# Kernel tuning notes

Measured on AMD Instinct MI355X. Metric: run time of the kernel, lower is better.

The kernel has to match this reference:

```python
import jax, jax.numpy as jnp
import numpy as np

B, L, DM = 4, 64, 1024
H, DK, DV = 16, 64, 64
D = H * DV            # 1024, selector feature dim
DI = 4096             # ffn hidden
NEG = -1.0e9


def _layer_norm(x, g, b, eps=1e-6):
    mu = jnp.mean(x, axis=-1, keepdims=True)
    var = jnp.mean((x - mu) ** 2, axis=-1, keepdims=True)
    return (x - mu) / jnp.sqrt(var + eps) * g + b


def setup_inputs() -> dict:
    key = jax.random.key(0)
    ks = jax.random.split(key, 20)
    s = 0.02
    inp = {
        'input_t': jax.random.normal(ks[0], (B, L, DM), jnp.float32),
        'input_a': jax.random.normal(ks[1], (B, L, DM), jnp.float32),
        'input_v': jax.random.normal(ks[2], (B, L, DM), jnp.float32),
        'mask': jnp.ones((B, L, L), jnp.int32),
        # attention projections (Linear without bias -> right-multiply matrices)
        'w_qs': jax.random.normal(ks[3], (DM, H * DK), jnp.float32) * s,
        'w_ks': jax.random.normal(ks[4], (DM, H * DK), jnp.float32) * s,
        'w_vs': jax.random.normal(ks[5], (DM, H * DV), jnp.float32) * s,
        'w_ds0': jax.random.normal(ks[6], (DM, D), jnp.float32) * s,
        'w_ds1': jax.random.normal(ks[7], (DM, D), jnp.float32) * s,
        # decision MLP dc: Linear(2D,2D) + ReLU + Linear(2D,2)
        'dc_w1': jax.random.normal(ks[8], (2 * D, 2 * D), jnp.float32) * s,
        'dc_b1': jnp.zeros((2 * D,), jnp.float32),
        'dc_w2': jax.random.normal(ks[9], (2 * D, 2), jnp.float32) * s,
        'dc_b2': jnp.zeros((2,), jnp.float32),
        'w_fc': jax.random.normal(ks[10], (H * DV, DM), jnp.float32) * s,
        'ln1_g': jnp.ones((DM,), jnp.float32),
        'ln1_b': jnp.zeros((DM,), jnp.float32),
        # shared positionwise FFN
        'ffn_w1': jax.random.normal(ks[11], (DM, DI), jnp.float32) * s,
        'ffn_b1': jnp.zeros((DI,), jnp.float32),
        'ffn_w2': jax.random.normal(ks[12], (DI, DM), jnp.float32) * s,
        'ffn_b2': jnp.zeros((DM,), jnp.float32),
        'ln2_g': jnp.ones((DM,), jnp.float32),
        'ln2_b': jnp.zeros((DM,), jnp.float32),
    }
    return inp


def _forward(input_t, input_a, input_v, mask, w_qs, w_ks, w_vs, w_ds0, w_ds1,
             dc_w1, dc_b1, dc_w2, dc_b2, w_fc, ln1_g, ln1_b,
             ffn_w1, ffn_b1, ffn_w2, ffn_b2, ln2_g, ln2_b):
    temp = DK ** 0.5
    lis = [input_t, input_a, input_v]
    nm = len(lis)
    mask4 = mask[:, None]  # [B,1,L,L], broadcast over heads
    outs = []
    for i in range(nm):  # query modality (fixed small loop)
        x = lis[i]
        residual = x
        d0 = x @ w_ds0                                      # [B,L,D]
        # f[b,q,k] = cat(d1[b,q], d0[b,k]); split dc_w1 rows to avoid [B,L,L,2D] input
        a0 = d0 @ dc_w1[D:]                                 # [B,L,2D] (key-index part)
        q = (x @ w_qs).reshape(B, L, H, DK).transpose(0, 2, 1, 3)  # [B,H,L,DK]
        attns, vs = [], []
        for j in range(nm):  # key/value modality
            y = lis[j]
            k = (y @ w_ks).reshape(B, L, H, DK).transpose(0, 2, 1, 3)
            v = (y @ w_vs).reshape(B, L, H, DV).transpose(0, 2, 1, 3)
            d1 = y @ w_ds1
            a1 = d1 @ dc_w1[:D]                              # [B,L,2D] (query-index part)
            hid = jax.nn.relu(a1[:, :, None, :] + a0[:, None, :, :] + dc_b1)  # [B,L,L,2D]
            logits = hid @ dc_w2 + dc_b2                     # [B,L,L,2]
            # gumbel_softmax, eval mode (no noise), tau=1, hard=True (straight-through)
            p = jax.nn.softmax(logits, axis=-1)
            y_soft = jax.nn.softmax(p, axis=-1)
            idx = jnp.argmax(y_soft, axis=-1)
            y_hard = jax.nn.one_hot(idx, 2, dtype=y_soft.dtype)
            ret = y_hard - jax.lax.stop_gradient(y_soft) + y_soft
            dec = ret[..., 1] * NEG                          # [B,L,L]
            attn = jnp.einsum('bhqd,bhkd->bhqk', q / temp, k) + dec[:, None]
            attn = jnp.where(mask4 == 0, NEG, attn)
            attns.append(attn)
            vs.append(v)
        A = jnp.stack(attns, axis=3).reshape(B, H, L, nm * L)  # [B,H,L,3L]
        A = jax.nn.softmax(A, axis=-1)
        V = jnp.stack(vs, axis=2).reshape(B, H, nm * L, DV)
        o = jnp.einsum('bhqk,bhkd->bhqd', A, V)
        o = o.transpose(0, 2, 1, 3).reshape(B, L, H * DV)
        o = o @ w_fc + residual
        o = _layer_norm(o, ln1_g, ln1_b)
        outs.append(o)
    # shared positionwise FFN applied to all modalities
    res = []
    for o in outs:
        h = jax.nn.relu(o @ ffn_w1 + ffn_b1) @ ffn_w2 + ffn_b2
        res.append(_layer_norm(h + o, ln2_g, ln2_b))
    return jnp.stack(res)  # [3,B,L,DM]


def reference(input_t, input_a, input_v, mask, w_qs, w_ks, w_vs, w_ds0, w_ds1,
              dc_w1, dc_b1, dc_w2, dc_b2, w_fc, ln1_g, ln1_b,
              ffn_w1, ffn_b1, ffn_w2, ffn_b2, ln2_g, ln2_b):
    return _forward(input_t, input_a, input_v, mask, w_qs, w_ks, w_vs, w_ds0, w_ds1,
                    dc_w1, dc_b1, dc_w2, dc_b2, w_fc, ln1_g, ln1_b,
                    ffn_w1, ffn_b1, ffn_w2, ffn_b2, ln2_g, ln2_b)
```

## Files before the change

kernel.cpp:

```cpp
#include <hip/hip_runtime.h>
#include <math.h>


#define NEGV (-1000000000.0f)

typedef float f32x4 __attribute__((ext_vector_type(4)));
typedef short short8 __attribute__((ext_vector_type(8)));
typedef unsigned short u16x8 __attribute__((ext_vector_type(8)));
typedef unsigned short u16x4 __attribute__((ext_vector_type(4)));

typedef __attribute__((address_space(1))) const void glob_cv;
typedef __attribute__((address_space(3))) void lds_v;

static __device__ __forceinline__ unsigned short f2bf(float f) {
  unsigned u = __builtin_bit_cast(unsigned, f);
  u += 0x7fffu + ((u >> 16) & 1u);
  return (unsigned short)(u >> 16);
}
static __device__ __forceinline__ float bf2f(unsigned short h) {
  return __builtin_bit_cast(float, ((unsigned)h) << 16);
}

static __device__ __forceinline__ void gload16(const unsigned short* g,
                                               unsigned short* l) {
  __builtin_amdgcn_global_load_lds((glob_cv*)g, (lds_v*)l, 16, 0, 0);
}

__global__ __launch_bounds__(256) void concat3(const float4* __restrict__ t,
                                               const float4* __restrict__ a,
                                               const float4* __restrict__ v,
                                               float4* __restrict__ Xf,
                                               u16x4* __restrict__ Xb) {
  int id = blockIdx.x * 256 + threadIdx.x;
  int m = id >> 16;
  int off = id & 65535;
  const float4* s = (m == 0) ? t : (m == 1) ? a : v;
  float4 val = s[off];
  Xf[id] = val;
  u16x4 bb;
  bb.x = f2bf(val.x); bb.y = f2bf(val.y);
  bb.z = f2bf(val.z); bb.w = f2bf(val.w);
  Xb[id] = bb;
}

struct WtJob { const float* src; unsigned short* dst; int K, N, tstart; };
struct WtJobs { WtJob j[9]; };

__global__ __launch_bounds__(256) void wt_transpose(WtJobs jobs) {
  __shared__ float Ls[32][33];
  int ji = 0;
#pragma unroll
  for (int t = 1; t < 9; ++t)
    if ((int)blockIdx.x >= jobs.j[t].tstart) ji = t;
  const WtJob jb = jobs.j[ji];
  int local = blockIdx.x - jb.tstart;
  int ntx = jb.N >> 5;
  int tk = local / ntx, tn = local - tk * ntx;
  const int tid = threadIdx.x;
  const int r = tid >> 3, c = (tid & 7) * 4;
  float4 v = *(const float4*)(jb.src + (size_t)(tk * 32 + r) * jb.N + tn * 32 + c);
  Ls[r][c + 0] = v.x; Ls[r][c + 1] = v.y;
  Ls[r][c + 2] = v.z; Ls[r][c + 3] = v.w;
  __syncthreads();
  u16x4 o;
  o.x = f2bf(Ls[c + 0][r]);
  o.y = f2bf(Ls[c + 1][r]);
  o.z = f2bf(Ls[c + 2][r]);
  o.w = f2bf(Ls[c + 3][r]);
  *(u16x4*)(jb.dst + (size_t)(tn * 32 + r) * jb.K + tk * 32 + c) = o;
}

struct GemmOp {
  const unsigned short* A;
  const unsigned short* B;
  const float* bias;
  const float* add;
  float* Cf;
  unsigned short* Cb;
  int lda, ldb, N, K, relu;
};
struct GemmBatch { GemmOp op[5]; };

__global__ __launch_bounds__(256, 2) void gemm_mfma(GemmBatch batch) {
  const GemmOp g = batch.op[blockIdx.z];
  __shared__ unsigned short As[64 * 64];
  __shared__ unsigned short Bs[128 * 64];
  const int bm = blockIdx.y * 64, bn = blockIdx.x * 128;
  const int tid = threadIdx.x;
  const int l = tid & 63, w = tid >> 6;
  const int wr = (w >> 1) * 32, wc = (w & 1) * 64;
  const int lr = l & 15, lg = l >> 4;
  const int crow = l >> 3;
  const int scol = ((l & 7) ^ (l >> 3)) * 8;
  const char* AsB = (const char*)As;
  const char* BsB = (const char*)Bs;
  f32x4 acc[2][4] = {};
  for (int k0 = 0; k0 < g.K; k0 += 64) {
    __syncthreads();
#pragma unroll
    for (int c = 0; c < 2; ++c) {
      const int ch = w * 2 + c;
      gload16(g.A + (size_t)(bm + ch * 8 + crow) * g.lda + k0 + scol,
              &As[ch * 512 + l * 8]);
    }
#pragma unroll
    for (int c = 0; c < 4; ++c) {
      const int ch = w * 4 + c;
      gload16(g.B + (size_t)(bn + ch * 8 + crow) * g.ldb + k0 + scol,
              &Bs[ch * 512 + l * 8]);
    }
    __syncthreads();
#pragma unroll
    for (int ks = 0; ks < 2; ++ks) {
      short8 af[2], bf[4];
#pragma unroll
      for (int i = 0; i < 2; ++i) {
        const int ra = wr + i * 16 + lr;
        af[i] = *(const short8*)(AsB +
                 ((ra * 128 + ks * 64 + lg * 16) ^ ((ra & 7) << 4)));
      }
#pragma unroll
      for (int j = 0; j < 4; ++j) {
        const int rb = wc + j * 16 + lr;
        bf[j] = *(const short8*)(BsB +
                 ((rb * 128 + ks * 64 + lg * 16) ^ ((rb & 7) << 4)));
      }
#pragma unroll
      for (int i = 0; i < 2; ++i)
#pragma unroll
        for (int j = 0; j < 4; ++j)
          acc[i][j] =
              __builtin_amdgcn_mfma_f32_16x16x32_bf16(af[i], bf[j], acc[i][j], 0, 0, 0);
    }
  }
#pragma unroll
  for (int j = 0; j < 4; ++j) {
    const int col = bn + wc + j * 16 + lr;
    const float bv = g.bias ? g.bias[col] : 0.0f;
#pragma unroll
    for (int i = 0; i < 2; ++i) {
#pragma unroll
      for (int ii = 0; ii < 4; ++ii) {
        const int row = bm + wr + i * 16 + lg * 4 + ii;
        float v = acc[i][j][ii] + bv;
        if (g.add) v += g.add[(size_t)row * g.N + col];
        if (g.relu) v = fmaxf(v, 0.0f);
        if (g.Cf) g.Cf[(size_t)row * g.N + col] = v;
        if (g.Cb) g.Cb[(size_t)row * g.N + col] = f2bf(v);
      }
    }
  }
}

__global__ __launch_bounds__(256) void decision_part(
    const float* __restrict__ A1, const float* __restrict__ A0,
    const float* __restrict__ w2, float* __restrict__ PART) {
  __shared__ float sA1[64][68];
  __shared__ float sA0[64][68];
  const int ds = blockIdx.x;
  const int b = blockIdx.y, pp = blockIdx.z;
  const int i = pp / 3, j = pp % 3;
  const int tid = threadIdx.x;
  const int tq = tid >> 4, tk = tid & 15;
  const float* a1base = A1 + ((size_t)(j * 4 + b) * 64) * 2048 + ds * 64;
  const float* a0base = A0 + ((size_t)(i * 4 + b) * 64) * 2048 + ds * 64;
#pragma unroll
  for (int t = 0; t < 4; ++t) {
    const int row = t * 16 + tq;
    const int col = tk * 4;
    *(float4*)&sA1[row][col] = *(const float4*)(a1base + (size_t)row * 2048 + col);
    *(float4*)&sA0[row][col] = *(const float4*)(a0base + (size_t)row * 2048 + col);
  }
  __syncthreads();
  float acc[4][4] = {};
  const float* wbase = w2 + (size_t)ds * 128;
#pragma unroll 4
  for (int s4 = 0; s4 < 16; ++s4) {
    float4 wv0 = *(const float4*)(wbase + s4 * 8);
    float4 wv1 = *(const float4*)(wbase + s4 * 8 + 4);
    float wd0 = wv0.y - wv0.x, wd1 = wv0.w - wv0.z;
    float wd2 = wv1.y - wv1.x, wd3 = wv1.w - wv1.z;
    float4 a1v[4], a0v[4];
#pragma unroll
    for (int r = 0; r < 4; ++r) {
      a1v[r] = *(const float4*)&sA1[tq + 16 * r][s4 * 4];
      a0v[r] = *(const float4*)&sA0[tk + 16 * r][s4 * 4];
    }
#pragma unroll
    for (int qr = 0; qr < 4; ++qr)
#pragma unroll
      for (int kr = 0; kr < 4; ++kr) {
        float a = acc[qr][kr];
        a = fmaf(fmaxf(a1v[qr].x + a0v[kr].x, 0.f), wd0, a);
        a = fmaf(fmaxf(a1v[qr].y + a0v[kr].y, 0.f), wd1, a);
        a = fmaf(fmaxf(a1v[qr].z + a0v[kr].z, 0.f), wd2, a);
        a = fmaf(fmaxf(a1v[qr].w + a0v[kr].w, 0.f), wd3, a);
        acc[qr][kr] = a;
      }
  }
  float* outp = PART + (size_t)ds * 147456 + ((size_t)pp * 4 + b) * 4096;
#pragma unroll
  for (int qr = 0; qr < 4; ++qr)
#pragma unroll
    for (int kr = 0; kr < 4; ++kr)
      outp[(tq + 16 * qr) * 64 + (tk + 16 * kr)] = acc[qr][kr];
}

__global__ __launch_bounds__(256) void decision_reduce(
    const float* __restrict__ PART, const float* __restrict__ b2,
    float* __restrict__ DEC) {
  const int out = blockIdx.x * 256 + threadIdx.x;
  float acc = 0.f;
#pragma unroll
  for (int s = 0; s < 32; ++s) acc += PART[(size_t)s * 147456 + out];
  const float thr = b2[0] - b2[1];
  DEC[out] = (acc > thr) ? NEGV : 0.f;
}

__global__ __launch_bounds__(256) void attn_mfma(
    const unsigned short* __restrict__ Qa, const unsigned short* __restrict__ Ka,
    const unsigned short* __restrict__ Va, const float* __restrict__ DEC,
    const int* __restrict__ mask, unsigned short* __restrict__ O) {
  __shared__ __align__(16) char sm[49408];
  char* KsP = sm;
  char* Vt = sm + 24576;
  float* invs = (float*)(sm + 49152);

  const int h = blockIdx.x, b = blockIdx.y, i = blockIdx.z;
  const int tid = threadIdx.x;
  const int l = tid & 63, w = tid >> 6;
  const int l15 = l & 15, lg = l >> 4;

#pragma unroll
  for (int rep = 0; rep < 6; ++rep) {
    int flat = rep * 256 + tid;
    int key = flat >> 3, c8 = flat & 7;
    int j = key >> 6, kl = key & 63;
    const size_t rowoff = (((size_t)(j * 4 + b) * 64 + kl) * 1024) + h * 64 + c8 * 8;
    u16x8 kv = *(const u16x8*)(Ka + rowoff);
    *(u16x8*)(KsP + ((key * 128 + c8 * 16) ^ ((key & 7) << 4))) = kv;
    u16x8 vv = *(const u16x8*)(Va + rowoff);
#pragma unroll
    for (int jj = 0; jj < 8; ++jj) {
      int d = c8 * 8 + jj;
      *(unsigned short*)(Vt + ((d * 384 + key * 2) ^ ((d & 7) << 4))) = vv[jj];
    }
  }

  const int qg = w * 16 + l15;
  const unsigned short* qsrc =
      Qa + (((size_t)(i * 4 + b) * 64 + qg) * 1024) + h * 64 + lg * 8;
  short8 qf0 = *(const short8*)(qsrc);
  short8 qf1 = *(const short8*)(qsrc + 32);

  __syncthreads();

  f32x4 s[12];
#pragma unroll
  for (int t = 0; t < 12; ++t) {
    const int key = t * 16 + l15;
    const int swz = (key & 7) << 4;
    short8 kf0 = *(const short8*)(KsP + ((key * 128 + 0 + lg * 16) ^ swz));
    short8 kf1 = *(const short8*)(KsP + ((key * 128 + 64 + lg * 16) ^ swz));
    f32x4 z = {0.f, 0.f, 0.f, 0.f};
    z = __builtin_amdgcn_mfma_f32_16x16x32_bf16(kf0, qf0, z, 0, 0, 0);
    z = __builtin_amdgcn_mfma_f32_16x16x32_bf16(kf1, qf1, z, 0, 0, 0);
    s[t] = z;
  }

  int mk[4][4];
#pragma unroll
  for (int t4 = 0; t4 < 4; ++t4)
#pragma unroll
    for (int r = 0; r < 4; ++r)
      mk[t4][r] = mask[((size_t)b * 64 + qg) * 64 + t4 * 16 + lg * 4 + r];

  float mx = -3.0e38f;
#pragma unroll
  for (int t = 0; t < 12; ++t) {
    const float* dbase =
        DEC + (((size_t)(i * 3 + (t >> 2)) * 4 + b) * 4096) + qg * 64;
#pragma unroll
    for (int r = 0; r < 4; ++r) {
      const int kl = (t & 3) * 16 + lg * 4 + r;
      float sv = s[t][r] * 0.125f + dbase[kl];
      if (mk[t & 3][r] == 0) sv = NEGV;
      s[t][r] = sv;
      mx = fmaxf(mx, sv);
    }
  }
  mx = fmaxf(mx, __shfl_xor(mx, 16));
  mx = fmaxf(mx, __shfl_xor(mx, 32));
  float sum = 0.f;
#pragma unroll
  for (int t = 0; t < 12; ++t)
#pragma unroll
    for (int r = 0; r < 4; ++r) {
      float p = __expf(s[t][r] - mx);
      s[t][r] = p;
      sum += p;
    }
  sum += __shfl_xor(sum, 16);
  sum += __shfl_xor(sum, 32);
  if (l < 16) invs[w * 16 + l] = 1.0f / sum;

  __syncthreads();

  char* Pmy = KsP + w * 6144;
  const int pswz = (l15 & 7) << 4;

#pragma unroll
  for (int t = 0; t < 12; ++t)
#pragma unroll
    for (int r = 0; r < 4; ++r) {
      const int key = t * 16 + lg * 4 + r;
      *(unsigned short*)(Pmy + ((l15 * 384 + key * 2) ^ pswz)) = f2bf(s[t][r]);
    }
  __syncthreads();

  f32x4 o[4] = {};
#pragma unroll
  for (int kc = 0; kc < 6; ++kc) {
    short8 pf = *(const short8*)(Pmy + ((l15 * 384 + kc * 64 + lg * 16) ^ pswz));
#pragma unroll
    for (int dt = 0; dt < 4; ++dt) {
      const int d = dt * 16 + l15;
      short8 vf = *(const short8*)(Vt + ((d * 384 + kc * 64 + lg * 16) ^ ((d & 7) << 4)));
      o[dt] = __builtin_amdgcn_mfma_f32_16x16x32_bf16(pf, vf, o[dt], 0, 0, 0);
    }
  }
  __syncthreads();

#pragma unroll
  for (int t = 0; t < 12; ++t)
#pragma unroll
    for (int r = 0; r < 4; ++r) {
      const int key = t * 16 + lg * 4 + r;
      float p = s[t][r];
      float lo = p - bf2f(f2bf(p));
      *(unsigned short*)(Pmy + ((l15 * 384 + key * 2) ^ pswz)) = f2bf(lo);
    }
  __syncthreads();

#pragma unroll
  for (int kc = 0; kc < 6; ++kc) {
    short8 pf = *(const short8*)(Pmy + ((l15 * 384 + kc * 64 + lg * 16) ^ pswz));
#pragma unroll
    for (int dt = 0; dt < 4; ++dt) {
      const int d = dt * 16 + l15;
      short8 vf = *(const short8*)(Vt + ((d * 384 + kc * 64 + lg * 16) ^ ((d & 7) << 4)));
      o[dt] = __builtin_amdgcn_mfma_f32_16x16x32_bf16(pf, vf, o[dt], 0, 0, 0);
    }
  }

#pragma unroll
  for (int dt = 0; dt < 4; ++dt)
#pragma unroll
    for (int r = 0; r < 4; ++r) {
      const int ql = lg * 4 + r;
      const float inv = invs[w * 16 + ql];
      const int d = dt * 16 + l15;
      O[(((size_t)(i * 4 + b) * 64 + w * 16 + ql) * 1024) + h * 64 + d] =
          f2bf(o[dt][r] * inv);
    }
}

__global__ __launch_bounds__(256) void ln_kernel(const float* __restrict__ X,
                                                 const float* __restrict__ g,
                                                 const float* __restrict__ be,
                                                 float* __restrict__ Y,
                                                 unsigned short* __restrict__ Yb) {
  __shared__ float rs[8];
  int row = blockIdx.x, tid = threadIdx.x;
  const float* x = X + (size_t)row * 1024 + tid * 4;
  float4 v = *(const float4*)x;
  float s = v.x + v.y + v.z + v.w;
  float s2 = v.x * v.x + v.y * v.y + v.z * v.z + v.w * v.w;
#pragma unroll
  for (int off = 32; off > 0; off >>= 1) {
    s += __shfl_down(s, off);
    s2 += __shfl_down(s2, off);
  }
  int lane = tid & 63, wid = tid >> 6;
  if (lane == 0) { rs[wid * 2] = s; rs[wid * 2 + 1] = s2; }
  __syncthreads();
  if (tid == 0) {
    float aa = rs[0] + rs[2] + rs[4] + rs[6];
    float cc = rs[1] + rs[3] + rs[5] + rs[7];
    rs[0] = aa; rs[1] = cc;
  }
  __syncthreads();
  float mu = rs[0] * (1.0f / 1024.0f);
  float var = rs[1] * (1.0f / 1024.0f) - mu * mu;
  var = fmaxf(var, 0.f);
  float inv = 1.0f / sqrtf(var + 1e-6f);
  float4 gv = *(const float4*)(g + tid * 4);
  float4 bv = *(const float4*)(be + tid * 4);
  float4 o;
  o.x = (v.x - mu) * inv * gv.x + bv.x;
  o.y = (v.y - mu) * inv * gv.y + bv.y;
  o.z = (v.z - mu) * inv * gv.z + bv.z;
  o.w = (v.w - mu) * inv * gv.w + bv.w;
  *(float4*)(Y + (size_t)row * 1024 + tid * 4) = o;
  if (Yb) {
    u16x4 ob;
    ob.x = f2bf(o.x); ob.y = f2bf(o.y); ob.z = f2bf(o.z); ob.w = f2bf(o.w);
    *(u16x4*)(Yb + (size_t)row * 1024 + tid * 4) = ob;
  }
}

__global__ __launch_bounds__(256) void fsum_ln(
    const float* __restrict__ P, const float* __restrict__ bias,
    const float* __restrict__ add, const float* __restrict__ g,
    const float* __restrict__ be, float* __restrict__ Y) {
  __shared__ float rs[8];
  int row = blockIdx.x, tid = threadIdx.x;
  const int c = tid * 4;
  const size_t o = (size_t)row * 1024 + c;
  float4 p0 = *(const float4*)(P + o);
  float4 p1 = *(const float4*)(P + 786432 + o);
  float4 p2 = *(const float4*)(P + 2 * 786432 + o);
  float4 p3 = *(const float4*)(P + 3 * 786432 + o);
  float4 bs = *(const float4*)(bias + c);
  float4 ad = *(const float4*)(add + o);
  float4 v;
  v.x = ((p0.x + p1.x) + (p2.x + p3.x)) + bs.x + ad.x;
  v.y = ((p0.y + p1.y) + (p2.y + p3.y)) + bs.y + ad.y;
  v.z = ((p0.z + p1.z) + (p2.z + p3.z)) + bs.z + ad.z;
  v.w = ((p0.w + p1.w) + (p2.w + p3.w)) + bs.w + ad.w;
  float s = v.x + v.y + v.z + v.w;
  float s2 = v.x * v.x + v.y * v.y + v.z * v.z + v.w * v.w;
#pragma unroll
  for (int off = 32; off > 0; off >>= 1) {
    s += __shfl_down(s, off);
    s2 += __shfl_down(s2, off);
  }
  int lane = tid & 63, wid = tid >> 6;
  if (lane == 0) { rs[wid * 2] = s; rs[wid * 2 + 1] = s2; }
  __syncthreads();
  if (tid == 0) {
    float aa = rs[0] + rs[2] + rs[4] + rs[6];
    float cc = rs[1] + rs[3] + rs[5] + rs[7];
    rs[0] = aa; rs[1] = cc;
  }
  __syncthreads();
  float mu = rs[0] * (1.0f / 1024.0f);
  float var = rs[1] * (1.0f / 1024.0f) - mu * mu;
  var = fmaxf(var, 0.f);
  float inv = 1.0f / sqrtf(var + 1e-6f);
  float4 gv = *(const float4*)(g + c);
  float4 bv = *(const float4*)(be + c);
  float4 r;
  r.x = (v.x - mu) * inv * gv.x + bv.x;
  r.y = (v.y - mu) * inv * gv.y + bv.y;
  r.z = (v.z - mu) * inv * gv.z + bv.z;
  r.w = (v.w - mu) * inv * gv.w + bv.w;
  *(float4*)(Y + o) = r;
}

extern "C" void kernel_launch(void* const* d_in, const int* in_sizes, int n_in,
                              void* d_out, int out_size, void* d_ws,
                              size_t ws_size, hipStream_t stream) {
  const float* in_t = (const float*)d_in[0];
  const float* in_a = (const float*)d_in[1];
  const float* in_v = (const float*)d_in[2];
  const int* mask = (const int*)d_in[3];
  const float* w_qs = (const float*)d_in[4];
  const float* w_ks = (const float*)d_in[5];
  const float* w_vs = (const float*)d_in[6];
  const float* w_ds0 = (const float*)d_in[7];
  const float* w_ds1 = (const float*)d_in[8];
  const float* dc_w1 = (const float*)d_in[9];
  const float* dc_b1 = (const float*)d_in[10];
  const float* dc_w2 = (const float*)d_in[11];
  const float* dc_b2 = (const float*)d_in[12];
  const float* w_fc = (const float*)d_in[13];
  const float* ln1_g = (const float*)d_in[14];
  const float* ln1_b = (const float*)d_in[15];
  const float* ffn_w1 = (const float*)d_in[16];
  const float* ffn_b1 = (const float*)d_in[17];
  const float* ffn_w2 = (const float*)d_in[18];
  const float* ffn_b2 = (const float*)d_in[19];
  const float* ln2_g = (const float*)d_in[20];
  const float* ln2_b = (const float*)d_in[21];
  float* out = (float*)d_out;

  char* p = (char*)d_ws;
  auto alloc = [&](size_t bytes) {
    char* r = p;
    p += (bytes + 255) & ~(size_t)255;
    return r;
  };
  unsigned short* WQS = (unsigned short*)alloc(1024 * 1024 * 2);
  unsigned short* WKS = (unsigned short*)alloc(1024 * 1024 * 2);
  unsigned short* WVS = (unsigned short*)alloc(1024 * 1024 * 2);
  unsigned short* WD0 = (unsigned short*)alloc(1024 * 1024 * 2);
  unsigned short* WD1 = (unsigned short*)alloc(1024 * 1024 * 2);
  unsigned short* WW1 = (unsigned short*)alloc((size_t)2048 * 2048 * 2);
  unsigned short* WFC = (unsigned short*)alloc(1024 * 1024 * 2);
  unsigned short* WF1 = (unsigned short*)alloc((size_t)4096 * 1024 * 2);
  unsigned short* WF2 = (unsigned short*)alloc((size_t)1024 * 4096 * 2);
  float* Xf = (float*)alloc((size_t)786432 * 4);
  unsigned short* Xb = (unsigned short*)alloc((size_t)786432 * 2);
  unsigned short* Qb = (unsigned short*)alloc((size_t)786432 * 2);
  unsigned short* Kb = (unsigned short*)alloc((size_t)786432 * 2);
  unsigned short* Vb = (unsigned short*)alloc((size_t)786432 * 2);
  unsigned short* D0b = (unsigned short*)alloc((size_t)786432 * 2);
  unsigned short* D1b = (unsigned short*)alloc((size_t)786432 * 2);
  float* DEC = (float*)alloc((size_t)147456 * 4);
  unsigned short* OATTb = (unsigned short*)alloc((size_t)786432 * 2);
  float* PART = (float*)alloc((size_t)32 * 147456 * 4);
  float* FPART = PART;
  char* U = alloc((size_t)14155776);
  float* A0f = (float*)U;
  float* A1f = (float*)(U + (size_t)6291456);
  float* F2 = (float*)U;
  float* O1f = (float*)(U + (size_t)3145728);
  unsigned short* O1b = (unsigned short*)(U + (size_t)6291456);
  unsigned short* Hfb = (unsigned short*)(U + (size_t)7864320);

  dim3 blk(256);

  WtJobs jobs;
  int ts = 0;
  auto setjob = [&](int idx, const float* s, unsigned short* d, int K, int N) {
    jobs.j[idx].src = s; jobs.j[idx].dst = d;
    jobs.j[idx].K = K; jobs.j[idx].N = N; jobs.j[idx].tstart = ts;
    ts += (K / 32) * (N / 32);
  };
  setjob(0, w_qs, WQS, 1024, 1024);
  setjob(1, w_ks, WKS, 1024, 1024);
  setjob(2, w_vs, WVS, 1024, 1024);
  setjob(3, w_ds0, WD0, 1024, 1024);
  setjob(4, w_ds1, WD1, 1024, 1024);
  setjob(5, dc_w1, WW1, 2048, 2048);
  setjob(6, w_fc, WFC, 1024, 1024);
  setjob(7, ffn_w1, WF1, 1024, 4096);
  setjob(8, ffn_w2, WF2, 4096, 1024);
  wt_transpose<<<dim3(ts), blk, 0, stream>>>(jobs);

  concat3<<<dim3(768), blk, 0, stream>>>((const float4*)in_t,
                                         (const float4*)in_a,
                                         (const float4*)in_v,
                                         (float4*)Xf, (u16x4*)Xb);

  GemmBatch proj{};
  unsigned short* pouts[5] = {Qb, Kb, Vb, D0b, D1b};
  const unsigned short* pws[5] = {WQS, WKS, WVS, WD0, WD1};
  for (int z = 0; z < 5; ++z) {
    proj.op[z].A = Xb; proj.op[z].B = pws[z];
    proj.op[z].bias = nullptr; proj.op[z].add = nullptr;
    proj.op[z].Cf = nullptr; proj.op[z].Cb = pouts[z];
    proj.op[z].lda = 1024; proj.op[z].ldb = 1024;
    proj.op[z].N = 1024; proj.op[z].K = 1024; proj.op[z].relu = 0;
  }
  gemm_mfma<<<dim3(8, 12, 5), blk, 0, stream>>>(proj);

  GemmBatch pair{};
  pair.op[0].A = D0b; pair.op[0].B = WW1 + 1024;
  pair.op[0].bias = nullptr; pair.op[0].add = nullptr;
  pair.op[0].Cf = A0f; pair.op[0].Cb = nullptr;
  pair.op[0].lda = 1024; pair.op[0].ldb = 2048;
  pair.op[0].N = 2048; pair.op[0].K = 1024; pair.op[0].relu = 0;
  pair.op[1] = pair.op[0];
  pair.op[1].A = D1b; pair.op[1].B = WW1; pair.op[1].bias = dc_b1;
  pair.op[1].Cf = A1f;
  gemm_mfma<<<dim3(16, 12, 2), blk, 0, stream>>>(pair);

  decision_part<<<dim3(32, 4, 9), blk, 0, stream>>>(A1f, A0f, dc_w2, PART);
  decision_reduce<<<dim3(576), blk, 0, stream>>>(PART, dc_b2, DEC);

  attn_mfma<<<dim3(16, 4, 3), blk, 0, stream>>>(Qb, Kb, Vb, DEC, mask, OATTb);

  GemmBatch fc{};
  fc.op[0].A = OATTb; fc.op[0].B = WFC;
  fc.op[0].bias = nullptr; fc.op[0].add = Xf;
  fc.op[0].Cf = F2; fc.op[0].Cb = nullptr;
  fc.op[0].lda = 1024; fc.op[0].ldb = 1024;
  fc.op[0].N = 1024; fc.op[0].K = 1024; fc.op[0].relu = 0;
  gemm_mfma<<<dim3(8, 12, 1), blk, 0, stream>>>(fc);

  ln_kernel<<<dim3(768), blk, 0, stream>>>(F2, ln1_g, ln1_b, O1f, O1b);

  GemmBatch f1{};
  f1.op[0].A = O1b; f1.op[0].B = WF1;
  f1.op[0].bias = ffn_b1; f1.op[0].add = nullptr;
  f1.op[0].Cf = nullptr; f1.op[0].Cb = Hfb;
  f1.op[0].lda = 1024; f1.op[0].ldb = 1024;
  f1.op[0].N = 4096; f1.op[0].K = 1024; f1.op[0].relu = 1;
  gemm_mfma<<<dim3(32, 12, 1), blk, 0, stream>>>(f1);

  GemmBatch f2{};
  for (int z = 0; z < 4; ++z) {
    f2.op[z].A = Hfb + (size_t)z * 1024;
    f2.op[z].B = WF2 + (size_t)z * 1024;
    f2.op[z].bias = nullptr; f2.op[z].add = nullptr;
    f2.op[z].Cf = FPART + (size_t)z * 786432; f2.op[z].Cb = nullptr;
    f2.op[z].lda = 4096; f2.op[z].ldb = 4096;
    f2.op[z].N = 1024; f2.op[z].K = 1024; f2.op[z].relu = 0;
  }
  gemm_mfma<<<dim3(8, 12, 4), blk, 0, stream>>>(f2);

  fsum_ln<<<dim3(768), blk, 0, stream>>>(FPART, ffn_b2, O1f, ln2_g, ln2_b, out);
}
```

Measured before the change: 163.0 us.

## Double-buffer GEMM LDS tiles and merge concat and weight transpose kernels

The GEMM kernel now keeps two LDS buffers and issues the global-to-LDS loads for the next K tile before computing on the current one, so memory latency overlaps with MFMA work and one barrier per iteration is dropped. The concat/bf16 cast kernel and the weight transpose kernel are merged into a single launch, removing one kernel launch. Doubling the LDS footprint to 48KB per block may reduce occupancy under the 2-blocks-per-CU launch bound.

```diff
diff --git a/kernel.cpp b/kernel.cpp
--- a/kernel.cpp
+++ b/kernel.cpp
@@ -26,41 +26,43 @@
   __builtin_amdgcn_global_load_lds((glob_cv*)g, (lds_v*)l, 16, 0, 0);
 }
 
-__global__ __launch_bounds__(256) void concat3(const float4* __restrict__ t,
-                                               const float4* __restrict__ a,
-                                               const float4* __restrict__ v,
-                                               float4* __restrict__ Xf,
-                                               u16x4* __restrict__ Xb) {
-  int id = blockIdx.x * 256 + threadIdx.x;
-  int m = id >> 16;
-  int off = id & 65535;
-  const float4* s = (m == 0) ? t : (m == 1) ? a : v;
-  float4 val = s[off];
-  Xf[id] = val;
-  u16x4 bb;
-  bb.x = f2bf(val.x); bb.y = f2bf(val.y);
-  bb.z = f2bf(val.z); bb.w = f2bf(val.w);
-  Xb[id] = bb;
-}
-
 struct WtJob { const float* src; unsigned short* dst; int K, N, tstart; };
 struct WtJobs { WtJob j[9]; };
 
-__global__ __launch_bounds__(256) void wt_transpose(WtJobs jobs) {
+__global__ __launch_bounds__(256) void prep(const float4* __restrict__ t,
+                                            const float4* __restrict__ a,
+                                            const float4* __restrict__ v,
+                                            float4* __restrict__ Xf,
+                                            u16x4* __restrict__ Xb,
+                                            WtJobs jobs) {
   __shared__ float Ls[32][33];
+  const int tid = threadIdx.x;
+  if (blockIdx.x < 768) {
+    int id = blockIdx.x * 256 + tid;
+    int m = id >> 16;
+    int off = id & 65535;
+    const float4* s = (m == 0) ? t : (m == 1) ? a : v;
+    float4 val = s[off];
+    Xf[id] = val;
+    u16x4 bb;
+    bb.x = f2bf(val.x); bb.y = f2bf(val.y);
+    bb.z = f2bf(val.z); bb.w = f2bf(val.w);
+    Xb[id] = bb;
+    return;
+  }
+  const int bx = blockIdx.x - 768;
   int ji = 0;
 #pragma unroll
-  for (int t = 1; t < 9; ++t)
-    if ((int)blockIdx.x >= jobs.j[t].tstart) ji = t;
+  for (int tj = 1; tj < 9; ++tj)
+    if (bx >= jobs.j[tj].tstart) ji = tj;
   const WtJob jb = jobs.j[ji];
-  int local = blockIdx.x - jb.tstart;
+  int local = bx - jb.tstart;
   int ntx = jb.N >> 5;
   int tk = local / ntx, tn = local - tk * ntx;
-  const int tid = threadIdx.x;
   const int r = tid >> 3, c = (tid & 7) * 4;
-  float4 v = *(const float4*)(jb.src + (size_t)(tk * 32 + r) * jb.N + tn * 32 + c);
-  Ls[r][c + 0] = v.x; Ls[r][c + 1] = v.y;
-  Ls[r][c + 2] = v.z; Ls[r][c + 3] = v.w;
+  float4 vv = *(const float4*)(jb.src + (size_t)(tk * 32 + r) * jb.N + tn * 32 + c);
+  Ls[r][c + 0] = vv.x; Ls[r][c + 1] = vv.y;
+  Ls[r][c + 2] = vv.z; Ls[r][c + 3] = vv.w;
   __syncthreads();
   u16x4 o;
   o.x = f2bf(Ls[c + 0][r]);
@@ -83,8 +85,8 @@
 
 __global__ __launch_bounds__(256, 2) void gemm_mfma(GemmBatch batch) {
   const GemmOp g = batch.op[blockIdx.z];
-  __shared__ unsigned short As[64 * 64];
-  __shared__ unsigned short Bs[128 * 64];
+  __shared__ unsigned short As[2][64 * 64];
+  __shared__ unsigned short Bs[2][128 * 64];
   const int bm = blockIdx.y * 64, bn = blockIdx.x * 128;
   const int tid = threadIdx.x;
   const int l = tid & 63, w = tid >> 6;
@@ -92,24 +94,41 @@
   const int lr = l & 15, lg = l >> 4;
   const int crow = l >> 3;
   const int scol = ((l & 7) ^ (l >> 3)) * 8;
-  const char* AsB = (const char*)As;
-  const char* BsB = (const char*)Bs;
+  const unsigned short* ap = g.A + (size_t)(bm + crow) * g.lda + scol;
+  const unsigned short* bp = g.B + (size_t)(bn + crow) * g.ldb + scol;
+
+#pragma unroll
+  for (int c = 0; c < 2; ++c) {
+    const int ch = w * 2 + c;
+    gload16(ap + (size_t)(ch * 8) * g.lda, &As[0][ch * 512 + l * 8]);
+  }
+#pragma unroll
+  for (int c = 0; c < 4; ++c) {
+    const int ch = w * 4 + c;
+    gload16(bp + (size_t)(ch * 8) * g.ldb, &Bs[0][ch * 512 + l * 8]);
+  }
+  __syncthreads();
+
   f32x4 acc[2][4] = {};
+  int cur = 0;
   for (int k0 = 0; k0 < g.K; k0 += 64) {
-    __syncthreads();
-#pragma unroll
-    for (int c = 0; c < 2; ++c) {
-      const int ch = w * 2 + c;
-      gload16(g.A + (size_t)(bm + ch * 8 + crow) * g.lda + k0 + scol,
-              &As[ch * 512 + l * 8]);
-    }
-#pragma unroll
-    for (int c = 0; c < 4; ++c) {
-      const int ch = w * 4 + c;
-      gload16(g.B + (size_t)(bn + ch * 8 + crow) * g.ldb + k0 + scol,
-              &Bs[ch * 512 + l * 8]);
-    }
-    __syncthreads();
+    if (k0 + 64 < g.K) {
+      const int nb = cur ^ 1;
+#pragma unroll
+      for (int c = 0; c < 2; ++c) {
+        const int ch = w * 2 + c;
+        gload16(ap + (size_t)(ch * 8) * g.lda + k0 + 64,
+                &As[nb][ch * 512 + l * 8]);
+      }
+#pragma unroll
+      for (int c = 0; c < 4; ++c) {
+        const int ch = w * 4 + c;
+        gload16(bp + (size_t)(ch * 8) * g.ldb + k0 + 64,
+                &Bs[nb][ch * 512 + l * 8]);
+      }
+    }
+    const char* AsB = (const char*)As[cur];
+    const char* BsB = (const char*)Bs[cur];
 #pragma unroll
     for (int ks = 0; ks < 2; ++ks) {
       short8 af[2], bf[4];
@@ -132,6 +151,8 @@
           acc[i][j] =
               __builtin_amdgcn_mfma_f32_16x16x32_bf16(af[i], bf[j], acc[i][j], 0, 0, 0);
     }
+    __syncthreads();
+    cur ^= 1;
   }
 #pragma unroll
   for (int j = 0; j < 4; ++j) {
@@ -537,12 +558,10 @@
   setjob(6, w_fc, WFC, 1024, 1024);
   setjob(7, ffn_w1, WF1, 1024, 4096);
   setjob(8, ffn_w2, WF2, 4096, 1024);
-  wt_transpose<<<dim3(ts), blk, 0, stream>>>(jobs);
-
-  concat3<<<dim3(768), blk, 0, stream>>>((const float4*)in_t,
-                                         (const float4*)in_a,
-                                         (const float4*)in_v,
-                                         (float4*)Xf, (u16x4*)Xb);
+  prep<<<dim3(768 + ts), blk, 0, stream>>>((const float4*)in_t,
+                                           (const float4*)in_a,
+                                           (const float4*)in_v,
+                                           (float4*)Xf, (u16x4*)Xb, jobs);
 
   GemmBatch proj{};
   unsigned short* pouts[5] = {Qb, Kb, Vb, D0b, D1b};
```

Result: no change. 166.2 us (+2.0%).
